# Kernel tuning notes

Measured on AMD Instinct MI355X. Metric: run time of the kernel, lower is better.

Reference implementation:

```python
import jax, jax.numpy as jnp
import numpy as np

N = 2048      # n_nodes
Q = 1024      # n_query
S = 512       # n_seeds
NBINS = 20
NPOWS = 5
HOP = 2


def _divide_no_nan(a, b):
    safe_b = jnp.where(b == 0, 1.0, b)
    return jnp.where(b == 0, 0.0, a / safe_b)


def _local_calib(g, calib_w):
    # soft-binning calibration: broadcast against NBINS Gaussian bumps
    parts = np.linspace(0.0, 1.0, NBINS)
    tmp = parts[1:] - parts[:-1]
    sig = np.zeros_like(parts)
    sig[:-1] += tmp
    sig[1:] += tmp
    sig[1:-1] /= 2.0
    sig = sig / 50.0  # sigma_div
    bases = jnp.asarray(parts, dtype=g.dtype)
    sigmas = jnp.asarray(sig, dtype=g.dtype)
    mask = (g > 0).astype(g.dtype)
    d = g[..., None] - bases            # [N, N, NBINS]
    z = jnp.exp(-(d * d) / sigmas)
    z = _divide_no_nan(z, jnp.sum(z, axis=-1, keepdims=True))
    probs = jax.nn.softmax(calib_w)     # use_cumsum=False
    out = jnp.sum(z * probs, axis=-1)
    return out * mask


def _normalize_by_degrees(g):
    # diag(1/sqrt(rowsum)) @ g @ diag(1/sqrt(colsum)), done as scaling
    dl = jnp.sqrt(jnp.sum(g, axis=1))
    dr = jnp.sqrt(jnp.sum(g, axis=0))
    left = _divide_no_nan(jnp.ones_like(dl), dl)
    right = _divide_no_nan(jnp.ones_like(dr), dr)
    return left[:, None] * g * right[None, :]


def _global_calib(g, w, b):
    # edge standardization + learned power series + elu shift
    mask = (g > 0).astype(g.dtype)
    n_nz = jnp.sum(mask)
    mean = jnp.sum(g) / n_nz
    d = g - mean
    var = jnp.sum(mask * d * d) / n_nz
    gn = (g - mean) / jnp.sqrt(var) * mask
    mult = jnp.abs(gn)
    mult_safe = jnp.where(mult == 0, 1.0, mult)
    sqr = jnp.where(mult == 0, 0.0, gn * jnp.sqrt(mult_safe) / mult_safe)
    powers = [gn, sqr]
    last = gn
    for _ in range(NPOWS - 2):
        last = last * mult
        powers.append(last)
    stacked = jnp.stack(powers, axis=-1)           # [Q, S, NPOWS]
    out = jnp.einsum('qsp,p->qs', stacked, w[:, 0]) + b[0]
    out = jax.nn.elu(out) + 1.0
    return out * mask


def setup_inputs() -> dict:
    key = jax.random.key(0)
    k1, k2, k3, k4, k5, k6 = jax.random.split(key, 6)
    u = jax.random.uniform(k1, (N, N), dtype=jnp.float32)
    sparsity = (jax.random.uniform(k2, (N, N)) > 0.5).astype(jnp.float32)
    graph = u * sparsity
    # CalibLocalLayer default init for calib_w
    parts = np.linspace(0.0, 1.0, NBINS)
    w_init = np.log(parts + 1e-06) - np.mean(parts)
    calib_w = jnp.asarray(w_init, dtype=jnp.float32)
    global_w = jnp.ones((NPOWS, 1), dtype=jnp.float32)
    global_b = jnp.zeros((1,), dtype=jnp.float32)
    # NodeImportanceLayer init from graph column degrees
    cw = np.array(_divide_no_nan(1.0, jnp.sqrt(jnp.sum(graph, axis=0))))
    cw = np.log(cw + 1e-06)
    cw = cw - np.mean(cw)
    col_weights = jnp.asarray(cw[None, :], dtype=jnp.float32)
    query_ids = jax.random.randint(k3, (Q,), 0, N, dtype=jnp.int32)
    seed_ids = jax.random.randint(k4, (S,), 0, N, dtype=jnp.int32)
    return {
        'graph': graph, 'calib_w': calib_w, 'global_w': global_w,
        'global_b': global_b, 'col_weights': col_weights,
        'query_ids': query_ids, 'seed_ids': seed_ids,
    }


def reference(graph, calib_w, global_w, global_b, col_weights, query_ids, seed_ids):
    n = graph.shape[0]
    g = _local_calib(graph, calib_w)               # calib_before_lp = 'local'
    g = _normalize_by_degrees(g)
    cw = jax.nn.softmax(col_weights, axis=1) * n   # node importance
    g = g * cw
    graph_mult = g
    gq = g[query_ids]                              # [Q, N]
    for _ in range(HOP - 1):
        gq = gq @ graph_mult                       # multi-hop propagation
    # zero self-edge: column j == query node id
    diag_mask = (jnp.arange(n)[None, :] != query_ids[:, None]).astype(gq.dtype)
    gq = gq * diag_mask
    gq = gq[:, seed_ids]                           # [Q, S]
    gq = _global_calib(gq, global_w, global_b)     # calib_after_lp = 'global'
    out = _divide_no_nan(gq, jnp.sum(gq, axis=1, keepdims=True))
    return out
```

## Files before the change

### kernel.cpp

```cpp
#include <hip/hip_runtime.h>
#include <hip/hip_bf16.h>

#define NDIM 2048
#define QDIM 1024
#define SDIM 512
#define NBINS 20
#define GT_TK 64
#define GT_TS 64
#define CAL_ROWS 4
#define NBLK1 (NDIM / CAL_ROWS)

typedef __attribute__((ext_vector_type(8))) short bf16x8;
typedef __attribute__((ext_vector_type(4))) float f32x4;

__device__ __forceinline__ unsigned short f2bf(float f) {
  unsigned int u = __builtin_bit_cast(unsigned int, f);
  u += 0x7fffu + ((u >> 16) & 1u);
  return (unsigned short)(u >> 16);
}
__device__ __forceinline__ float bf2f(unsigned short h) {
  return __builtin_bit_cast(float, (unsigned int)h << 16);
}
__device__ __forceinline__ float guard_rsqrt(float x) {
  return x > 0.f ? 1.0f / sqrtf(x) : 0.f;
}

__global__ __launch_bounds__(256) void k_calib(const float* __restrict__ graph,
                                               const float* __restrict__ calib_w,
                                               unsigned short* __restrict__ g0bf,
                                               float* __restrict__ rowsum,
                                               float* __restrict__ colpart) {
  __shared__ float sp[NBINS];
  __shared__ float lrowp[CAL_ROWS][4];
  int t = threadIdx.x;
  if (t == 0) {
    float m = -1e30f;
    for (int b = 0; b < NBINS; b++) m = fmaxf(m, calib_w[b]);
    float e[NBINS]; float s = 0.f;
    for (int b = 0; b < NBINS; b++) { e[b] = __expf(calib_w[b] - m); s += e[b]; }
    float inv = 1.0f / s;
    for (int b = 0; b < NBINS; b++) sp[b] = e[b] * inv;
  }
  __syncthreads();
  const float q1 = __expf(-950.0f / 361.0f);
  const float q2 = __expf(-950.0f * 4.0f / 361.0f);
  const float q3 = __expf(-950.0f * 9.0f / 361.0f);
  const float q4 = __expf(-950.0f * 16.0f / 361.0f);
  int r0 = blockIdx.x * CAL_ROWS;
  float colacc[8] = {0.f,0.f,0.f,0.f,0.f,0.f,0.f,0.f};
  #pragma unroll
  for (int r = 0; r < CAL_ROWS; r++) {
    int row = r0 + r;
    const float4* src = (const float4*)(graph + (size_t)row * NDIM);
    float4 in0 = src[t * 2];
    float4 in1 = src[t * 2 + 1];
    float gv[8] = {in0.x, in0.y, in0.z, in0.w, in1.x, in1.y, in1.z, in1.w};
    unsigned short ov[8];
    float rs = 0.f;
    #pragma unroll
    for (int i = 0; i < 8; i++) {
      float g = gv[i];
      float v = 0.f;
      if (g > 0.f) {
        int bstar = (int)floorf(g * 19.0f + 0.5f);
        int lo = bstar - 2;
        lo = lo < 0 ? 0 : (lo > NBINS - 5 ? NBINS - 5 : lo);
        float delta = g - (float)lo * (1.0f / 19.0f);
        float rr = __expf(100.0f * delta);
        float r2_ = rr * rr;
        float r3_ = r2_ * rr;
        float r4_ = r2_ * r2_;
        float den = 1.0f + q1 * rr + q2 * r2_ + q3 * r3_ + q4 * r4_;
        float num = sp[lo] + q1 * rr * sp[lo+1] + q2 * r2_ * sp[lo+2]
                  + q3 * r3_ * sp[lo+3] + q4 * r4_ * sp[lo+4];
        v = num / den;
      }
      ov[i] = f2bf(v);
      rs += v;
      colacc[i] += v;
    }
    uint4 packed;
    __builtin_memcpy(&packed, ov, 16);
    *(uint4*)(g0bf + (size_t)row * NDIM + t * 8) = packed;
    #pragma unroll
    for (int m = 32; m > 0; m >>= 1) rs += __shfl_xor(rs, m);
    if ((t & 63) == 0) lrowp[r][t >> 6] = rs;
  }
  float* cp = colpart + (size_t)blockIdx.x * NDIM + t * 8;
  *(float4*)cp       = *(float4*)&colacc[0];
  *(float4*)(cp + 4) = *(float4*)&colacc[4];
  __syncthreads();
  if (t < CAL_ROWS) rowsum[r0 + t] = lrowp[t][0] + lrowp[t][1] + lrowp[t][2] + lrowp[t][3];
}

__global__ __launch_bounds__(256) void k_colreduce(const float* __restrict__ colpart,
                                                   float* __restrict__ colsum) {
  __shared__ float red[4][64];
  int t = threadIdx.x;
  int c = blockIdx.x * 64 + (t & 63);
  int p0 = (t >> 6) * 128;
  float s = 0.f;
  #pragma unroll 8
  for (int p = 0; p < 128; p++)
    s += colpart[(size_t)(p0 + p) * NDIM + c];
  red[t >> 6][t & 63] = s;
  __syncthreads();
  if (t < 64)
    colsum[blockIdx.x * 64 + t] = red[0][t] + red[1][t] + red[2][t] + red[3][t];
}

__global__ __launch_bounds__(512) void k_gatherBt(const unsigned short* __restrict__ g0bf,
                                                  const int* __restrict__ sid,
                                                  const float* __restrict__ rowsum,
                                                  const float* __restrict__ colsum,
                                                  const float* __restrict__ col_w,
                                                  unsigned short* __restrict__ Bt) {
  __shared__ int scol[GT_TS];
  __shared__ float lrsc[GT_TS];
  __shared__ float lmv[GT_TK];
  __shared__ unsigned short lt[GT_TS][GT_TK + 4];
  int t = threadIdx.x;
  int k0 = blockIdx.x * GT_TK;
  int s0 = blockIdx.y * GT_TS;
  if (t < GT_TS) {
    int col = sid[s0 + t];
    scol[t] = col;
    lrsc[t] = guard_rsqrt(colsum[col]) * __expf(col_w[col]);
  } else if (t < GT_TS + GT_TK) {
    int k = k0 + t - GT_TS;
    lmv[t - GT_TS] = guard_rsqrt(rowsum[k]) * guard_rsqrt(colsum[k]) * __expf(col_w[k]);
  }
  __syncthreads();
  int tx = t & 63;
  int ty = t >> 6;
  #pragma unroll
  for (int r = ty; r < GT_TK; r += 8) {
    float v = bf2f(g0bf[(size_t)(k0 + r) * NDIM + scol[tx]]);
    lt[tx][r] = f2bf(v * lmv[r] * lrsc[tx]);
  }
  __syncthreads();
  int s = t >> 3;
  int kk = (t & 7) * 8;
  uint4 val;
  __builtin_memcpy(&val, &lt[s][kk], 16);
  *(uint4*)(Bt + (size_t)(s0 + s) * NDIM + k0 + kk) = val;
}

__global__ __launch_bounds__(256) void k_mfma_stats(const unsigned short* __restrict__ g0bf,
                                                    const unsigned short* __restrict__ Bt,
                                                    const int* __restrict__ qid,
                                                    const int* __restrict__ sid,
                                                    const float* __restrict__ rowsum,
                                                    float* __restrict__ C,
                                                    double* __restrict__ stats_s,
                                                    double* __restrict__ stats_s2,
                                                    double* __restrict__ stats_c) {
  __shared__ float lacc[4][32 * 33];
  __shared__ float r1[256], r2[256]; __shared__ int rc[256];
  int t = threadIdx.x;
  int lane = t & 63, wave = t >> 6;
  int n0 = blockIdx.x * 32;
  int m0 = blockIdx.y * 32;
  int fr = lane & 15;
  int kq = (lane >> 4) * 8;
  int kbase = wave * 512;
  int qa0 = qid[m0 + fr];
  int qa1 = qid[m0 + 16 + fr];
  const unsigned short* Ap0 = g0bf + (size_t)qa0 * NDIM + kbase + kq;
  const unsigned short* Ap1 = g0bf + (size_t)qa1 * NDIM + kbase + kq;
  const unsigned short* Bp0 = Bt + (size_t)(n0 + fr) * NDIM + kbase + kq;
  const unsigned short* Bp1 = Bp0 + (size_t)16 * NDIM;
  f32x4 acc00 = {0.f,0.f,0.f,0.f}, acc01 = acc00, acc10 = acc00, acc11 = acc00;
  #pragma unroll 4
  for (int i = 0; i < 16; i++) {
    int off = i * 32;
    bf16x8 a0 = *(const bf16x8*)(Ap0 + off);
    bf16x8 a1 = *(const bf16x8*)(Ap1 + off);
    bf16x8 b0 = *(const bf16x8*)(Bp0 + off);
    bf16x8 b1 = *(const bf16x8*)(Bp1 + off);
    acc00 = __builtin_amdgcn_mfma_f32_16x16x32_bf16(a0, b0, acc00, 0, 0, 0);
    acc01 = __builtin_amdgcn_mfma_f32_16x16x32_bf16(a0, b1, acc01, 0, 0, 0);
    acc10 = __builtin_amdgcn_mfma_f32_16x16x32_bf16(a1, b0, acc10, 0, 0, 0);
    acc11 = __builtin_amdgcn_mfma_f32_16x16x32_bf16(a1, b1, acc11, 0, 0, 0);
  }
  int r0_ = (lane >> 4) * 4;
  int c0_ = lane & 15;
  float* L = lacc[wave];
  #pragma unroll
  for (int r = 0; r < 4; r++) {
    L[(r0_ + r) * 33 + c0_]            = acc00[r];
    L[(r0_ + r) * 33 + 16 + c0_]       = acc01[r];
    L[(16 + r0_ + r) * 33 + c0_]       = acc10[r];
    L[(16 + r0_ + r) * 33 + 16 + c0_]  = acc11[r];
  }
  __syncthreads();
  float s = 0.f, s2 = 0.f; int c = 0;
  #pragma unroll
  for (int e = t; e < 1024; e += 256) {
    int row = e >> 5, col = e & 31;
    int li = row * 33 + col;
    float v = lacc[0][li] + lacc[1][li] + lacc[2][li] + lacc[3][li];
    int mrow = m0 + row;
    int qv = qid[mrow];
    v *= guard_rsqrt(rowsum[qv]);
    if (sid[n0 + col] == qv) v = 0.f;
    C[(size_t)mrow * SDIM + n0 + col] = v;
    if (v > 0.f) { s += v; s2 += v * v; c++; }
  }
  r1[t] = s; r2[t] = s2; rc[t] = c; __syncthreads();
  for (int st = 128; st > 0; st >>= 1) {
    if (t < st) { r1[t] += r1[t+st]; r2[t] += r2[t+st]; rc[t] += rc[t+st]; }
    __syncthreads();
  }
  if (t == 0) {
    int sidx = blockIdx.y * 16 + blockIdx.x;
    stats_s[sidx]  = (double)r1[0];
    stats_s2[sidx] = (double)r2[0];
    stats_c[sidx]  = (double)rc[0];
  }
}

__global__ void k_final(const float* __restrict__ C,
                        const double* __restrict__ stats_s,
                        const double* __restrict__ stats_s2,
                        const double* __restrict__ stats_c,
                        const float* __restrict__ gw, const float* __restrict__ gb,
                        float* __restrict__ out) {
  __shared__ double d1[256], d2[256], d3[256];
  __shared__ float red[256];
  int q = blockIdx.x, t = threadIdx.x;
  d1[t] = stats_s[t]  + stats_s[t + 256];
  d2[t] = stats_s2[t] + stats_s2[t + 256];
  d3[t] = stats_c[t]  + stats_c[t + 256];
  __syncthreads();
  for (int st = 128; st > 0; st >>= 1) {
    if (t < st) { d1[t] += d1[t+st]; d2[t] += d2[t+st]; d3[t] += d3[t+st]; }
    __syncthreads();
  }
  double mean_d = d1[0] / d3[0];
  double var_d = d2[0] / d3[0] - mean_d * mean_d;
  float mean = (float)mean_d;
  float invstd = (float)(1.0 / sqrt(var_d));
  float w0 = gw[0], w1 = gw[1], w2 = gw[2], w3 = gw[3], w4 = gw[4], bb = gb[0];
  float vals[2]; float rs = 0.f;
  #pragma unroll
  for (int p = 0; p < 2; p++) {
    int s = t + p * 256;
    float x = C[(size_t)q * SDIM + s];
    float v = 0.f;
    if (x > 0.f) {
      float gn = (x - mean) * invstd;
      float m = fabsf(gn);
      float sgnsq = (m > 0.f) ? (gn / m) * sqrtf(m) : 0.f;
      float acc = w0 * gn + w1 * sgnsq;
      float gm = gn * m; acc += w2 * gm;
      gm *= m;           acc += w3 * gm;
      gm *= m;           acc += w4 * gm;
      acc += bb;
      v = (acc > 0.f ? acc : __expf(acc) - 1.f) + 1.f;
    }
    vals[p] = v; rs += v;
  }
  red[t] = rs; __syncthreads();
  for (int st = 128; st > 0; st >>= 1) { if (t < st) red[t] += red[t+st]; __syncthreads(); }
  float tot = red[0];
  float inv = tot > 0.f ? 1.0f / tot : 0.f;
  #pragma unroll
  for (int p = 0; p < 2; p++) {
    int s = t + p * 256;
    out[(size_t)q * SDIM + s] = vals[p] * inv;
  }
}

extern "C" void kernel_launch(void* const* d_in, const int* in_sizes, int n_in,
                              void* d_out, int out_size, void* d_ws, size_t ws_size,
                              hipStream_t stream) {
  const float* graph    = (const float*)d_in[0];
  const float* calib_w  = (const float*)d_in[1];
  const float* global_w = (const float*)d_in[2];
  const float* global_b = (const float*)d_in[3];
  const float* col_w    = (const float*)d_in[4];
  const int*   qid      = (const int*)d_in[5];
  const int*   sid      = (const int*)d_in[6];
  float* out = (float*)d_out;

  char* ws = (char*)d_ws;
  float*  colsum   = (float*)(ws + 0);
  float*  rowsum   = (float*)(ws + 8192);
  double* stats_s  = (double*)(ws + 16384);
  double* stats_s2 = (double*)(ws + 20480);
  double* stats_c  = (double*)(ws + 24576);
  unsigned short* g0bf = (unsigned short*)(ws + 65536);
  unsigned short* Bt   = (unsigned short*)(ws + 65536 + 8388608);
  float*  C      = (float*)(ws + 65536 + 8388608 + 2097152);
  float*  colpart = (float*)(ws + 65536 + 8388608 + 2097152 + 2097152);

  k_calib<<<NBLK1, 256, 0, stream>>>(graph, calib_w, g0bf, rowsum, colpart);
  k_colreduce<<<NDIM / 64, 256, 0, stream>>>(colpart, colsum);
  k_gatherBt<<<dim3(NDIM / GT_TK, SDIM / GT_TS), 512, 0, stream>>>(g0bf, sid, rowsum, colsum, col_w, Bt);
  k_mfma_stats<<<dim3(SDIM / 32, QDIM / 32), 256, 0, stream>>>(g0bf, Bt, qid, sid, rowsum, C, stats_s, stats_s2, stats_c);
  k_final<<<QDIM, 256, 0, stream>>>(C, stats_s, stats_s2, stats_c, global_w, global_b, out);
}
```

Baseline: 118.9 us.

## Stage full row tiles in LDS for seed-column gather and widen colreduce grid

k_gatherBt now loads 32 full rows of the bf16 graph into shared memory with coalesced 16-byte loads. Each thread then builds its seed column's 32-element K-slice from LDS and writes it as four 16-byte stores. This replaces scattered 2-byte global gathers per seed column. k_colreduce is re-split into 64 blocks of 32 columns with 8 partial groups to increase parallelism. The 128KB LDS tile allows only one block per CU, and the grid is just 64 blocks, so occupancy and parallelism are reduced.

```diff
diff --git a/kernel.cpp b/kernel.cpp
--- a/kernel.cpp
+++ b/kernel.cpp
@@ -5,10 +5,9 @@
 #define QDIM 1024
 #define SDIM 512
 #define NBINS 20
-#define GT_TK 64
-#define GT_TS 64
 #define CAL_ROWS 4
 #define NBLK1 (NDIM / CAL_ROWS)
+#define K2_KT 32
 
 typedef __attribute__((ext_vector_type(8))) short bf16x8;
 typedef __attribute__((ext_vector_type(4))) float f32x4;
@@ -95,55 +94,67 @@
 
 __global__ __launch_bounds__(256) void k_colreduce(const float* __restrict__ colpart,
                                                    float* __restrict__ colsum) {
-  __shared__ float red[4][64];
+  __shared__ float red[8][32];
   int t = threadIdx.x;
-  int c = blockIdx.x * 64 + (t & 63);
-  int p0 = (t >> 6) * 128;
+  int c = blockIdx.x * 32 + (t & 31);
+  int p0 = (t >> 5) * 64;
   float s = 0.f;
   #pragma unroll 8
-  for (int p = 0; p < 128; p++)
+  for (int p = 0; p < 64; p++)
     s += colpart[(size_t)(p0 + p) * NDIM + c];
-  red[t >> 6][t & 63] = s;
-  __syncthreads();
-  if (t < 64)
-    colsum[blockIdx.x * 64 + t] = red[0][t] + red[1][t] + red[2][t] + red[3][t];
-}
-
-__global__ __launch_bounds__(512) void k_gatherBt(const unsigned short* __restrict__ g0bf,
+  red[t >> 5][t & 31] = s;
+  __syncthreads();
+  if (t < 32) {
+    float v = 0.f;
+    #pragma unroll
+    for (int g = 0; g < 8; g++) v += red[g][t];
+    colsum[blockIdx.x * 32 + t] = v;
+  }
+}
+
+__global__ __launch_bounds__(256) void k_gatherBt(const unsigned short* __restrict__ g0bf,
                                                   const int* __restrict__ sid,
                                                   const float* __restrict__ rowsum,
                                                   const float* __restrict__ colsum,
                                                   const float* __restrict__ col_w,
                                                   unsigned short* __restrict__ Bt) {
-  __shared__ int scol[GT_TS];
-  __shared__ float lrsc[GT_TS];
-  __shared__ float lmv[GT_TK];
-  __shared__ unsigned short lt[GT_TS][GT_TK + 4];
+  __shared__ unsigned short rows[K2_KT * NDIM];
+  __shared__ int scol[SDIM];
+  __shared__ float lrsc[SDIM];
+  __shared__ float lmv[K2_KT];
   int t = threadIdx.x;
-  int k0 = blockIdx.x * GT_TK;
-  int s0 = blockIdx.y * GT_TS;
-  if (t < GT_TS) {
-    int col = sid[s0 + t];
-    scol[t] = col;
-    lrsc[t] = guard_rsqrt(colsum[col]) * __expf(col_w[col]);
-  } else if (t < GT_TS + GT_TK) {
-    int k = k0 + t - GT_TS;
-    lmv[t - GT_TS] = guard_rsqrt(rowsum[k]) * guard_rsqrt(colsum[k]) * __expf(col_w[k]);
-  }
-  __syncthreads();
-  int tx = t & 63;
-  int ty = t >> 6;
-  #pragma unroll
-  for (int r = ty; r < GT_TK; r += 8) {
-    float v = bf2f(g0bf[(size_t)(k0 + r) * NDIM + scol[tx]]);
-    lt[tx][r] = f2bf(v * lmv[r] * lrsc[tx]);
-  }
-  __syncthreads();
-  int s = t >> 3;
-  int kk = (t & 7) * 8;
-  uint4 val;
-  __builtin_memcpy(&val, &lt[s][kk], 16);
-  *(uint4*)(Bt + (size_t)(s0 + s) * NDIM + k0 + kk) = val;
+  int k0 = blockIdx.x * K2_KT;
+  for (int i = t; i < SDIM; i += 256) {
+    int col = sid[i];
+    scol[i] = col;
+    lrsc[i] = guard_rsqrt(colsum[col]) * __expf(col_w[col]);
+  }
+  if (t < K2_KT) {
+    int k = k0 + t;
+    lmv[t] = guard_rsqrt(rowsum[k]) * guard_rsqrt(colsum[k]) * __expf(col_w[k]);
+  }
+  for (int r = 0; r < K2_KT; r++) {
+    *(uint4*)&rows[r * NDIM + t * 8] =
+        *(const uint4*)(g0bf + (size_t)(k0 + r) * NDIM + t * 8);
+  }
+  __syncthreads();
+  for (int sv = t; sv < SDIM; sv += 256) {
+    int c = scol[sv];
+    float rs = lrsc[sv];
+    unsigned short ov[K2_KT];
+    #pragma unroll
+    for (int k = 0; k < K2_KT; k++) {
+      float v = bf2f(rows[k * NDIM + c]);
+      ov[k] = f2bf(v * lmv[k] * rs);
+    }
+    uint4 w0, w1, w2, w3;
+    __builtin_memcpy(&w0, &ov[0], 16);
+    __builtin_memcpy(&w1, &ov[8], 16);
+    __builtin_memcpy(&w2, &ov[16], 16);
+    __builtin_memcpy(&w3, &ov[24], 16);
+    uint4* dst = (uint4*)(Bt + (size_t)sv * NDIM + k0);
+    dst[0] = w0; dst[1] = w1; dst[2] = w2; dst[3] = w3;
+  }
 }
 
 __global__ __launch_bounds__(256) void k_mfma_stats(const unsigned short* __restrict__ g0bf,
@@ -296,8 +307,8 @@
   float*  colpart = (float*)(ws + 65536 + 8388608 + 2097152 + 2097152);
 
   k_calib<<<NBLK1, 256, 0, stream>>>(graph, calib_w, g0bf, rowsum, colpart);
-  k_colreduce<<<NDIM / 64, 256, 0, stream>>>(colpart, colsum);
-  k_gatherBt<<<dim3(NDIM / GT_TK, SDIM / GT_TS), 512, 0, stream>>>(g0bf, sid, rowsum, colsum, col_w, Bt);
+  k_colreduce<<<64, 256, 0, stream>>>(colpart, colsum);
+  k_gatherBt<<<NDIM / K2_KT, 256, 0, stream>>>(g0bf, sid, rowsum, colsum, col_w, Bt);
   k_mfma_stats<<<dim3(SDIM / 32, QDIM / 32), 256, 0, stream>>>(g0bf, Bt, qid, sid, rowsum, C, stats_s, stats_s2, stats_c);
   k_final<<<QDIM, 256, 0, stream>>>(C, stats_s, stats_s2, stats_c, global_w, global_b, out);
 }
```

New measurement: 118.8 us. No clear change (-0.1%).
